# Performance work log

Measured on AMD Instinct MI355X. Metric: run time of the kernel, lower is better.

## Reference

```python
import jax, jax.numpy as jnp
import numpy as np

B, T, F, V, NTXT = 32, 1, 1, 729, 64
DIM, DIM_LLM = 1152, 4096
HEADS, DIM_HEAD, DEPTH, NUM_LATENTS, FF_MULT = 16, 96, 6, 64, 4
INNER = HEADS * DIM_HEAD
FF_INNER = DIM * FF_MULT
SCALE = DIM_HEAD ** -0.5


def _ln(x, w, b, eps=1e-5):
    mu = x.mean(-1, keepdims=True)
    var = ((x - mu) ** 2).mean(-1, keepdims=True)
    return (x - mu) * jax.lax.rsqrt(var + eps) * w + b


def setup_inputs() -> dict:
    key = jax.random.key(0)
    ks = jax.random.split(key, 12)
    w = lambda k, shape: jax.random.normal(k, shape, dtype=jnp.float32) * 0.02
    return {
        "x": jax.random.normal(ks[0], (B, T, F, V, DIM), dtype=jnp.float32),
        "text_embeds": jax.random.normal(ks[1], (B, NTXT, DIM_LLM), dtype=jnp.float32),
        "latents": jax.random.normal(ks[2], (NUM_LATENTS, DIM), dtype=jnp.float32),
        "txt_w1": w(ks[3], (DIM_LLM, DIM)),
        "txt_b1": jnp.zeros((DIM,), jnp.float32),
        "txt_w2": w(ks[4], (DIM, DIM)),
        "txt_b2": jnp.zeros((DIM,), jnp.float32),
        "nm_w": jnp.ones((DEPTH, DIM), jnp.float32),
        "nm_b": jnp.zeros((DEPTH, DIM), jnp.float32),
        "nl_w": jnp.ones((DEPTH, DIM), jnp.float32),
        "nl_b": jnp.zeros((DEPTH, DIM), jnp.float32),
        "Wq": w(ks[5], (DEPTH, DIM, INNER)),
        "Wkv": w(ks[6], (DEPTH, DIM, 2 * INNER)),
        "Wo": w(ks[7], (DEPTH, INNER, DIM)),
        "ffln_w": jnp.ones((DEPTH, DIM), jnp.float32),
        "ffln_b": jnp.zeros((DEPTH, DIM), jnp.float32),
        "ff_w1": w(ks[8], (DEPTH, DIM, FF_INNER)),
        "ff_w2": w(ks[9], (DEPTH, FF_INNER, DIM)),
        "out_ln_w": jnp.ones((DIM,), jnp.float32),
        "out_ln_b": jnp.zeros((DIM,), jnp.float32),
    }


def reference(x, text_embeds, latents, txt_w1, txt_b1, txt_w2, txt_b2,
              nm_w, nm_b, nl_w, nl_b, Wq, Wkv, Wo,
              ffln_w, ffln_b, ff_w1, ff_w2, out_ln_w, out_ln_b):
    b, t, f, v, d = x.shape
    xf = x.reshape(b, t, f * v, d)  # (b, T, F*v, D)
    # text_projection: Linear -> GELU -> Linear
    txt = jax.nn.gelu(text_embeds @ txt_w1 + txt_b1, approximate=False) @ txt_w2 + txt_b2
    lat = jnp.broadcast_to(latents, (b, t, NUM_LATENTS, d))
    lat = jnp.concatenate(
        [lat, jnp.broadcast_to(txt[:, None], (b, t, txt.shape[1], d))], axis=2)
    n2 = lat.shape[2]
    for i in range(DEPTH):
        # PerceiverAttention
        xm = _ln(xf, nm_w[i], nm_b[i])
        lm = _ln(lat, nl_w[i], nl_b[i])
        q = (lm @ Wq[i]).reshape(b, t, n2, HEADS, DIM_HEAD)
        kv = jnp.concatenate([xm, lm], axis=2) @ Wkv[i]
        k, v_ = jnp.split(kv, 2, axis=-1)
        nk = k.shape[2]
        k = k.reshape(b, t, nk, HEADS, DIM_HEAD)
        v_ = v_.reshape(b, t, nk, HEADS, DIM_HEAD)
        sim = jnp.einsum('btihd,btjhd->bthij', q * SCALE, k)
        attn = jax.nn.softmax(sim, axis=-1)  # stable softmax == amax subtract + softmax
        out = jnp.einsum('bthij,btjhd->btihd', attn, v_).reshape(b, t, n2, INNER) @ Wo[i]
        lat = out + lat
        # FeedForward: LN -> Linear -> GELU -> Linear, residual
        lat = jax.nn.gelu(_ln(lat, ffln_w[i], ffln_b[i]) @ ff_w1[i],
                          approximate=False) @ ff_w2[i] + lat
    lat = lat[:, :, :NUM_LATENTS, :]
    return _ln(lat, out_ln_w, out_ln_b)
```

## Files before the change

### kernel.cpp

```cpp
#include <hip/hip_runtime.h>
#include <hip/hip_bf16.h>
#include <math.h>


typedef __attribute__((ext_vector_type(4))) float f32x4;
typedef __attribute__((ext_vector_type(8))) short bf16x8;
typedef unsigned int u32;

#define DEV __device__ __forceinline__

DEV float bf2f(short s){ union{u32 u; float f;} v; v.u = ((u32)(unsigned short)s) << 16; return v.f; }
DEV short f2bf(float f){
  union{float f; u32 u;} v; v.f = f;
  u32 r = (v.u + 0x7FFFu + ((v.u >> 16) & 1u)) >> 16;
  return (short)r;
}

DEV u32 lds_off(const short* p){
  return (u32)(uintptr_t)(__attribute__((address_space(3))) const short*)p;
}
template<int OFF>
DEV bf16x8 dsro(u32 addr){
  bf16x8 r;
  asm volatile("ds_read_b128 %0, %1 offset:%2" : "=v"(r) : "v"(addr), "i"(OFF));
  return r;
}

template<int GELU, int BIAS, int OUTF32, int CMAP, int KSPLIT>
__global__ __launch_bounds__(512, 4)
void gemm_v2(const short* __restrict__ A, const short* __restrict__ Bm,
             void* __restrict__ Cv, short* __restrict__ C2,
             const float* __restrict__ bias,
             int K, int lda, int ldb, int ldc,
             int Mvalid, int NBmax, int Nwrite)
{
  __shared__ __align__(16) short LDS[36864];

  int Mb = gridDim.x;
  int nwg = gridDim.x * gridDim.y;
  int bid = blockIdx.y * gridDim.x + blockIdx.x;
  int m0, n0;
  if ((Mb & 7) == 0){
    int mslab = Mb >> 3;
    int c = bid & 7, s = bid >> 3;
    int ml = s % mslab, nl = s / mslab;
    m0 = (c*mslab + ml) * 128;
    n0 = nl * 256;
  } else if ((nwg & 7) == 0){
    int chunk = nwg >> 3;
    int b2 = (bid & 7)*chunk + (bid >> 3);
    int by = b2 / Mb;
    m0 = (b2 - by*Mb) * 128;
    n0 = by * 256;
  } else {
    m0 = blockIdx.x * 128;
    n0 = blockIdx.y * 256;
  }
  int kzoff = KSPLIT ? (int)blockIdx.z * K : 0;

  int tid = threadIdx.x, lane = tid & 63, w = tid >> 6;
  int wr = w >> 2, wc = w & 3;
  int rsel = lane & 15, g4 = lane >> 4;

  int sl = lane >> 3;
  int l  = (lane & 7) ^ sl;
  int lc = (l & 3) * 8;
  int lh = l >> 2;
  const short* gA;
  { int r = m0 + w*8 + sl + lh*64; if (r > Mvalid-1) r = Mvalid-1;
    gA = A + (long)r*lda + lc + kzoff; }
  const short* gB0;
  { int r = n0 + w*8 + sl + lh*128; if (r > NBmax-1) r = NBmax-1;
    gB0 = Bm + (long)r*ldb + lc + kzoff; }
  const short* gB1;
  { int r = n0 + 64 + w*8 + sl + lh*128; if (r > NBmax-1) r = NBmax-1;
    gB1 = Bm + (long)r*ldb + lc + kzoff; }
  char* dA  = (char*)LDS + w*1024;
  char* dB0 = (char*)LDS + 8192  + w*1024;
  char* dB1 = (char*)LDS + 16384 + w*1024;

#define GLDS(src, dst) __builtin_amdgcn_global_load_lds( \
      (const __attribute__((address_space(1))) u32*)(src), \
      (__attribute__((address_space(3))) u32*)(dst), 16, 0, 0)
#define STAGE(bo, tau) do { \
    int kb = (tau)*32; \
    GLDS(gA  + kb, dA  + (bo)); \
    GLDS(gB0 + kb, dB0 + (bo)); \
    GLDS(gB1 + kb, dB1 + (bo)); \
  } while(0)

  u32 base = lds_off(LDS);
  u32 aAddr = base + (u32)(rsel*128 + (((wr*4 + g4) ^ (rsel & 7))*16));
  u32 bAddr = base + 8192u
            + (u32)(((wc & 1)*64 + rsel)*128 + ((((wc >> 1)*4 + g4) ^ (rsel & 7))*16));

  int nt = K >> 5;

  f32x4 acc[4][4];
#pragma unroll
  for (int i=0;i<4;i++)
#pragma unroll
    for (int j=0;j<4;j++) acc[i][j] = (f32x4){0.f,0.f,0.f,0.f};

  STAGE(0u, 0);
  if (nt > 1) STAGE(24576u, 1);

  u32 boCur = 0;
#pragma unroll 1
  for (int t=0; t<nt; ++t){
    if (t == nt-1) { asm volatile("s_waitcnt vmcnt(0)" ::: "memory"); }
    else           { asm volatile("s_waitcnt vmcnt(3)" ::: "memory"); }
    asm volatile("s_barrier" ::: "memory");
    u32 aa = aAddr + boCur, bb = bAddr + boCur;
    bf16x8 af[4], bfr[4];
    af[0]  = dsro<0>(aa);    af[1]  = dsro<2048>(aa);
    af[2]  = dsro<4096>(aa); af[3]  = dsro<6144>(aa);
    bfr[0] = dsro<0>(bb);    bfr[1] = dsro<2048>(bb);
    bfr[2] = dsro<4096>(bb); bfr[3] = dsro<6144>(bb);
    if (t+2 < nt){
      u32 boN2 = boCur + 49152u; if (boN2 >= 73728u) boN2 -= 73728u;
      STAGE(boN2, t+2);
    }
    asm volatile("s_waitcnt lgkmcnt(0)" ::: "memory");
    __builtin_amdgcn_sched_barrier(0);
    __builtin_amdgcn_s_setprio(1);
#pragma unroll
    for (int mi=0; mi<4; mi++)
#pragma unroll
      for (int nn=0; nn<4; nn++)
        acc[mi][nn] = __builtin_amdgcn_mfma_f32_16x16x32_bf16(af[mi], bfr[nn], acc[mi][nn], 0, 0, 0);
    __builtin_amdgcn_s_setprio(0);
    boCur += 24576u; if (boCur == 73728u) boCur = 0;
  }
#undef STAGE
#undef GLDS

  int cq = g4 * 4;
  int csel = rsel;
#pragma unroll
  for (int mi=0; mi<4; mi++){
#pragma unroll
    for (int nn=0; nn<4; nn++){
#pragma unroll
      for (int j=0; j<4; j++){
        int gm = m0 + wr*64 + mi*16 + cq + j;
        int gn = n0 + wc*64 + nn*16 + csel;
        if (gm < Mvalid && gn < Nwrite){
          float v = acc[mi][nn][j];
          if (BIAS) v += bias[gn];
          if (GELU) v = 0.5f*v*(1.0f + erff(v*0.70710678118654752f));
          if (CMAP == 0){
            long off = (long)gm*ldc + gn;
            if (KSPLIT) off += (long)blockIdx.z * ((long)Mvalid * ldc);
            if (OUTF32) ((float*)Cv)[off] = v;
            else        ((short*)Cv)[off] = f2bf(v);
          } else if (CMAP == 1){
            int bb2 = gm / 729;
            int jj = gm - bb2*729;
            ((short*)Cv)[((long)bb2*857 + jj)*3072 + gn] = f2bf(v);
          } else {
            if (gn < 1536){
              ((short*)Cv)[(long)gm*1536 + gn] = f2bf(v * 0.1020620726159657f);
            } else {
              int bb2 = gm >> 7, jj = gm & 127;
              C2[((long)bb2*857 + 729 + jj)*3072 + (gn - 1536)] = f2bf(v);
            }
          }
        }
      }
    }
  }
}

__global__ __launch_bounds__(512, 4)
void gemm_qkvx(const short* __restrict__ lm, const short* __restrict__ xnorm,
               const short* __restrict__ wTq, const short* __restrict__ wTx,
               short* __restrict__ qb, short* __restrict__ kv,
               const float* __restrict__ biasL)
{
  __shared__ __align__(16) short LDS[36864];

  int bid = blockIdx.x;
  int which = (bid >= 576);
  const short* A; const short* Bm;
  int m0, n0, Mvalid, NBmax;
  if (!which){
    int mslab = 4;
    int c = bid & 7, s = bid >> 3;
    m0 = (c*mslab + s % mslab) * 128;
    n0 = (s / mslab) * 256;
    A = lm; Bm = wTq; Mvalid = 4096; NBmax = 4608;
  } else {
    int local = bid - 576;
    int mslab = 23;
    int c = local & 7, s = local >> 3;
    m0 = (c*mslab + s % mslab) * 128;
    n0 = (s / mslab) * 256;
    A = xnorm; Bm = wTx; Mvalid = 23328; NBmax = 3072;
  }

  int tid = threadIdx.x, lane = tid & 63, w = tid >> 6;
  int wr = w >> 2, wc = w & 3;
  int rsel = lane & 15, g4 = lane >> 4;

  int sl = lane >> 3;
  int l  = (lane & 7) ^ sl;
  int lc = (l & 3) * 8;
  int lh = l >> 2;
  const short* gA;
  { int r = m0 + w*8 + sl + lh*64; if (r > Mvalid-1) r = Mvalid-1;
    gA = A + (long)r*1152 + lc; }
  const short* gB0;
  { int r = n0 + w*8 + sl + lh*128; if (r > NBmax-1) r = NBmax-1;
    gB0 = Bm + (long)r*1152 + lc; }
  const short* gB1;
  { int r = n0 + 64 + w*8 + sl + lh*128; if (r > NBmax-1) r = NBmax-1;
    gB1 = Bm + (long)r*1152 + lc; }
  char* dA  = (char*)LDS + w*1024;
  char* dB0 = (char*)LDS + 8192  + w*1024;
  char* dB1 = (char*)LDS + 16384 + w*1024;

#define GLDS(src, dst) __builtin_amdgcn_global_load_lds( \
      (const __attribute__((address_space(1))) u32*)(src), \
      (__attribute__((address_space(3))) u32*)(dst), 16, 0, 0)
#define STAGE(bo, tau) do { \
    int kb = (tau)*32; \
    GLDS(gA  + kb, dA  + (bo)); \
    GLDS(gB0 + kb, dB0 + (bo)); \
    GLDS(gB1 + kb, dB1 + (bo)); \
  } while(0)

  u32 base = lds_off(LDS);
  u32 aAddr = base + (u32)(rsel*128 + (((wr*4 + g4) ^ (rsel & 7))*16));
  u32 bAddr = base + 8192u
            + (u32)(((wc & 1)*64 + rsel)*128 + ((((wc >> 1)*4 + g4) ^ (rsel & 7))*16));

  const int nt = 36;

  f32x4 acc[4][4];
#pragma unroll
  for (int i=0;i<4;i++)
#pragma unroll
    for (int j=0;j<4;j++) acc[i][j] = (f32x4){0.f,0.f,0.f,0.f};

  STAGE(0u, 0);
  STAGE(24576u, 1);

  u32 boCur = 0;
#pragma unroll 1
  for (int t=0; t<nt; ++t){
    if (t == nt-1) { asm volatile("s_waitcnt vmcnt(0)" ::: "memory"); }
    else           { asm volatile("s_waitcnt vmcnt(3)" ::: "memory"); }
    asm volatile("s_barrier" ::: "memory");
    u32 aa = aAddr + boCur, bb = bAddr + boCur;
    bf16x8 af[4], bfr[4];
    af[0]  = dsro<0>(aa);    af[1]  = dsro<2048>(aa);
    af[2]  = dsro<4096>(aa); af[3]  = dsro<6144>(aa);
    bfr[0] = dsro<0>(bb);    bfr[1] = dsro<2048>(bb);
    bfr[2] = dsro<4096>(bb); bfr[3] = dsro<6144>(bb);
    if (t+2 < nt){
      u32 boN2 = boCur + 49152u; if (boN2 >= 73728u) boN2 -= 73728u;
      STAGE(boN2, t+2);
    }
    asm volatile("s_waitcnt lgkmcnt(0)" ::: "memory");
    __builtin_amdgcn_sched_barrier(0);
    __builtin_amdgcn_s_setprio(1);
#pragma unroll
    for (int mi=0; mi<4; mi++)
#pragma unroll
      for (int nn=0; nn<4; nn++)
        acc[mi][nn] = __builtin_amdgcn_mfma_f32_16x16x32_bf16(af[mi], bfr[nn], acc[mi][nn], 0, 0, 0);
    __builtin_amdgcn_s_setprio(0);
    boCur += 24576u; if (boCur == 73728u) boCur = 0;
  }
#undef STAGE
#undef GLDS

  int cq = g4 * 4;
  int csel = rsel;
#pragma unroll
  for (int mi=0; mi<4; mi++){
#pragma unroll
    for (int nn=0; nn<4; nn++){
#pragma unroll
      for (int j=0; j<4; j++){
        int gm = m0 + wr*64 + mi*16 + cq + j;
        int gn = n0 + wc*64 + nn*16 + csel;
        if (!which){
          if (gm < 4096 && gn < 4608){
            float v = acc[mi][nn][j];
            if (gn < 1536){
              qb[(long)gm*1536 + gn] = f2bf(v * 0.1020620726159657f);
            } else {
              int bb2 = gm >> 7, jj = gm & 127;
              kv[((long)bb2*857 + 729 + jj)*3072 + (gn - 1536)] = f2bf(v);
            }
          }
        } else {
          if (gm < 23328 && gn < 3072){
            float v = acc[mi][nn][j] + biasL[gn];
            int bb2 = gm / 729;
            int jj = gm - bb2*729;
            kv[((long)bb2*857 + jj)*3072 + gn] = f2bf(v);
          }
        }
      }
    }
  }
}

__global__ __launch_bounds__(256)
void red2_ln(float* __restrict__ lat, const float* __restrict__ p, long n,
             short* __restrict__ lm, const float* __restrict__ w,
             const float* __restrict__ b)
{
  const int D = 1152;
  int r = blockIdx.x;
  long rb = (long)r*D;
  int tid = threadIdx.x;
  float s1=0.f, s2=0.f;
  float xv[5];
#pragma unroll
  for (int t=0;t<5;t++){
    int i = tid + t*256;
    float v = 0.f;
    if (i < D){
      v = lat[rb+i] + p[rb+i] + p[n+rb+i];
      lat[rb+i] = v;
    }
    xv[t] = v; s1 += v; s2 += v*v;
  }
  if (!w) return;
#pragma unroll
  for (int o=32;o;o>>=1){ s1 += __shfl_xor(s1,o); s2 += __shfl_xor(s2,o); }
  __shared__ float red[8];
  int wid = tid>>6, lane = tid&63;
  if (lane==0){ red[wid]=s1; red[4+wid]=s2; }
  __syncthreads();
  s1 = red[0]+red[1]+red[2]+red[3];
  s2 = red[4]+red[5]+red[6]+red[7];
  float mu = s1 / D;
  float var = s2 / D - mu*mu;
  float rs = rsqrtf(var + 1e-5f);
#pragma unroll
  for (int t=0;t<5;t++){
    int i = tid + t*256;
    if (i >= D) break;
    lm[rb+i] = f2bf((xv[t]-mu)*rs*w[i] + b[i]);
  }
}

__global__ __launch_bounds__(256)
void flash_attn(const short* __restrict__ qb, const short* __restrict__ kv,
                short* __restrict__ attn)
{
  __shared__ short Kt[96][104];
  __shared__ short Vs[96][104];
  __shared__ short Pb[4][32][104];
  __shared__ float FAC[128];

  int z = blockIdx.x;
  int b = z >> 4, h = z & 15;
  int tid = threadIdx.x;
  int lane = tid & 63;
  int w = tid >> 6;
  int l15 = lane & 15, g4 = lane >> 4;

  bf16x8 qf[2][3];
#pragma unroll
  for (int n=0;n<2;n++)
#pragma unroll
    for (int kf=0;kf<3;kf++)
      qf[n][kf] = *(const bf16x8*)&qb[((long)(b*128 + w*32 + n*16 + l15))*1536
                                     + h*96 + kf*32 + g4*8];

  f32x4 acc[2][6];
#pragma unroll
  for (int i=0;i<2;i++)
#pragma unroll
    for (int j=0;j<6;j++) acc[i][j] = (f32x4){0.f,0.f,0.f,0.f};
  float m_run[2] = {-1e30f, -1e30f};
  float l_run[2] = {0.f, 0.f};

  const short* kvb = kv + (long)b*857*3072 + h*96;
  const short* vvb = kvb + 1536;

  for (int t=0; t<9; ++t){
    int k0 = t*96;
    for (int c = tid; c < 1152; c += 256){
      int r = c / 12;
      int c12 = c - r*12;
      int key = k0 + r; if (key > 856) key = 856;
      *(bf16x8*)&Kt[r][c12*8] = *(const bf16x8*)&kvb[(long)key*3072 + c12*8];
      bf16x8 vv = *(const bf16x8*)&vvb[(long)key*3072 + c12*8];
#pragma unroll
      for (int j=0;j<8;j++) Vs[c12*8 + j][r] = ((short*)&vv)[j];
    }
    __syncthreads();

    f32x4 st[6][2];
#pragma unroll
    for (int m=0;m<6;m++){ st[m][0]=(f32x4){0,0,0,0}; st[m][1]=(f32x4){0,0,0,0}; }
#pragma unroll
    for (int kf=0;kf<3;kf++){
      bf16x8 af[6];
#pragma unroll
      for (int m=0;m<6;m++) af[m] = *(const bf16x8*)&Kt[m*16 + l15][kf*32 + g4*8];
#pragma unroll
      for (int m=0;m<6;m++){
        st[m][0] = __builtin_amdgcn_mfma_f32_16x16x32_bf16(af[m], qf[0][kf], st[m][0], 0,0,0);
        st[m][1] = __builtin_amdgcn_mfma_f32_16x16x32_bf16(af[m], qf[1][kf], st[m][1], 0,0,0);
      }
    }

    if (k0 + 96 > 857){
#pragma unroll
      for (int m=0;m<6;m++)
#pragma unroll
        for (int j=0;j<4;j++){
          if (k0 + m*16 + g4*4 + j > 856){ st[m][0][j] = -1e30f; st[m][1][j] = -1e30f; }
        }
    }

#pragma unroll
    for (int n=0;n<2;n++){
      float mx = -1e30f;
#pragma unroll
      for (int m=0;m<6;m++)
#pragma unroll
        for (int j=0;j<4;j++) mx = fmaxf(mx, st[m][n][j]);
      mx = fmaxf(mx, __shfl_xor(mx, 16));
      mx = fmaxf(mx, __shfl_xor(mx, 32));
      float mn = fmaxf(m_run[n], mx);
      float f  = __expf(m_run[n] - mn);
      m_run[n] = mn;
      float s = 0.f;
#pragma unroll
      for (int m=0;m<6;m++)
#pragma unroll
        for (int j=0;j<4;j++){
          float e = __expf(st[m][n][j] - mn);
          st[m][n][j] = e; s += e;
        }
      s += __shfl_xor(s, 16);
      s += __shfl_xor(s, 32);
      l_run[n] = l_run[n]*f + s;
      if (g4 == 0) FAC[w*32 + n*16 + l15] = f;
    }

#pragma unroll
    for (int m=0;m<6;m++)
#pragma unroll
      for (int n=0;n<2;n++){
        short4 pk;
        pk.x = f2bf(st[m][n][0]); pk.y = f2bf(st[m][n][1]);
        pk.z = f2bf(st[m][n][2]); pk.w = f2bf(st[m][n][3]);
        *(short4*)&Pb[w][n*16 + l15][m*16 + g4*4] = pk;
      }

    {
      float4 fj0 = *(const float4*)&FAC[w*32 +  0 + g4*4];
      float4 fj1 = *(const float4*)&FAC[w*32 + 16 + g4*4];
#pragma unroll
      for (int nn=0;nn<6;nn++){
        acc[0][nn][0] *= fj0.x; acc[0][nn][1] *= fj0.y;
        acc[0][nn][2] *= fj0.z; acc[0][nn][3] *= fj0.w;
        acc[1][nn][0] *= fj1.x; acc[1][nn][1] *= fj1.y;
        acc[1][nn][2] *= fj1.z; acc[1][nn][3] *= fj1.w;
      }
    }

#pragma unroll
    for (int kf=0;kf<3;kf++){
      bf16x8 pa0 = *(const bf16x8*)&Pb[w][ 0 + l15][kf*32 + g4*8];
      bf16x8 pa1 = *(const bf16x8*)&Pb[w][16 + l15][kf*32 + g4*8];
#pragma unroll
      for (int nn=0;nn<6;nn++){
        bf16x8 vb = *(const bf16x8*)&Vs[nn*16 + l15][kf*32 + g4*8];
        acc[0][nn] = __builtin_amdgcn_mfma_f32_16x16x32_bf16(pa0, vb, acc[0][nn], 0,0,0);
        acc[1][nn] = __builtin_amdgcn_mfma_f32_16x16x32_bf16(pa1, vb, acc[1][nn], 0,0,0);
      }
    }
    __syncthreads();
  }

  if (g4 == 0){
    FAC[w*32 +  0 + l15] = 1.0f / l_run[0];
    FAC[w*32 + 16 + l15] = 1.0f / l_run[1];
  }
  float4 li0 = *(const float4*)&FAC[w*32 +  0 + g4*4];
  float4 li1 = *(const float4*)&FAC[w*32 + 16 + g4*4];
  float li[2][4] = {{li0.x,li0.y,li0.z,li0.w},{li1.x,li1.y,li1.z,li1.w}};
#pragma unroll
  for (int mo=0;mo<2;mo++)
#pragma unroll
    for (int nn=0;nn<6;nn++)
#pragma unroll
      for (int j=0;j<4;j++){
        int q = w*32 + mo*16 + g4*4 + j;
        int d = nn*16 + l15;
        attn[((long)(b*128+q))*1536 + h*96 + d] = f2bf(acc[mo][nn][j]*li[mo][j]);
      }
}

template<int GELU, int BIAS, int RES, int OUTF32>
__global__ __launch_bounds__(256)
void gemm_t(const short* __restrict__ A, const short* __restrict__ B,
            void* __restrict__ C, const float* __restrict__ bias,
            const float* __restrict__ res,
            int K, int lda, int ldb, int ldc,
            int Mvalid, int NBmax, int Nwrite,
            int zdiv, long sA1, long sA2, long sB1, long sB2, long sC1, long sC2,
            float scale)
{
  __shared__ __align__(16) short As[2][128*32];
  __shared__ __align__(16) short Bs[2][128*32];

  int z = blockIdx.z;
  int zq = z / zdiv, zr = z - zq*zdiv;
  const short* Ab = A + zq*sA1 + zr*sA2;
  const short* Bb = B + zq*sB1 + zr*sB2;
  long cOff = zq*sC1 + zr*sC2;
  int m0 = blockIdx.y * 128;
  int n0 = blockIdx.x * 128;
  int tid = threadIdx.x;
  int lane = tid & 63;
  int w = tid >> 6;
  int wm = (w >> 1) * 64, wn = (w & 1) * 64;

  int sr = lane >> 2;
  int sc = (lane & 3) * 8;
  int ar0 = m0 + w*32 + sr;
  int br0 = n0 + w*32 + sr;

  int raA0 = ar0;      if (raA0 > Mvalid-1) raA0 = Mvalid-1;
  int raA1 = ar0 + 16; if (raA1 > Mvalid-1) raA1 = Mvalid-1;
  int rbB0 = br0;      if (rbB0 > NBmax-1) rbB0 = NBmax-1;
  int rbB1 = br0 + 16; if (rbB1 > NBmax-1) rbB1 = NBmax-1;
  const short* gA0 = Ab + (long)raA0*lda + sc;
  const short* gA1 = Ab + (long)raA1*lda + sc;
  const short* gB0 = Bb + (long)rbB0*ldb + sc;
  const short* gB1 = Bb + (long)rbB1*ldb + sc;
  int ldsRow0 = (w*32)*32;
  int ldsRow1 = (w*32 + 16)*32;

  f32x4 acc[4][4];
#pragma unroll
  for (int i=0;i<4;i++)
#pragma unroll
    for (int j=0;j<4;j++) acc[i][j] = (f32x4){0.f,0.f,0.f,0.f};

  auto stage = [&](int buf, int kb){
    __builtin_amdgcn_global_load_lds(
        (const __attribute__((address_space(1))) u32*)(gA0 + kb),
        (__attribute__((address_space(3))) u32*)(&As[buf][ldsRow0]), 16, 0, 0);
    __builtin_amdgcn_global_load_lds(
        (const __attribute__((address_space(1))) u32*)(gA1 + kb),
        (__attribute__((address_space(3))) u32*)(&As[buf][ldsRow1]), 16, 0, 0);
    __builtin_amdgcn_global_load_lds(
        (const __attribute__((address_space(1))) u32*)(gB0 + kb),
        (__attribute__((address_space(3))) u32*)(&Bs[buf][ldsRow0]), 16, 0, 0);
    __builtin_amdgcn_global_load_lds(
        (const __attribute__((address_space(1))) u32*)(gB1 + kb),
        (__attribute__((address_space(3))) u32*)(&Bs[buf][ldsRow1]), 16, 0, 0);
  };

  int nt = K >> 5;
  stage(0, 0);
  __syncthreads();

  int kq = (lane >> 4) * 8;
  int rsel = lane & 15;
  int cur = 0;
  for (int t = 0; t < nt; ++t){
    if (t + 1 < nt) stage(cur ^ 1, (t+1)*32);

    bf16x8 af[4], bfr[4];
#pragma unroll
    for (int m=0;m<4;m++) af[m]  = *(const bf16x8*)&As[cur][(wm + m*16 + rsel)*32 + kq];
#pragma unroll
    for (int n=0;n<4;n++) bfr[n] = *(const bf16x8*)&Bs[cur][(wn + n*16 + rsel)*32 + kq];
#pragma unroll
    for (int m=0;m<4;m++)
#pragma unroll
      for (int n=0;n<4;n++)
        acc[m][n] = __builtin_amdgcn_mfma_f32_16x16x32_bf16(af[m], bfr[n], acc[m][n], 0, 0, 0);

    __syncthreads();
    cur ^= 1;
  }

  int cq = (lane >> 4) * 4;
  int csel = lane & 15;
#pragma unroll
  for (int m=0;m<4;m++){
#pragma unroll
    for (int n=0;n<4;n++){
#pragma unroll
      for (int j=0;j<4;j++){
        int gm = m0 + wm + m*16 + cq + j;
        int gn = n0 + wn + n*16 + csel;
        if (gm < Mvalid && gn < Nwrite){
          float v = acc[m][n][j] * scale;
          if (BIAS) v += bias[gn];
          if (GELU) v = 0.5f*v*(1.0f + erff(v*0.70710678118654752f));
          long off = cOff + (long)gm*ldc + gn;
          if (OUTF32){
            float rv = RES ? res[off] : 0.0f;
            ((float*)C)[off] = v + rv;
          } else {
            ((short*)C)[off] = f2bf(v);
          }
        }
      }
    }
  }
}

__global__ __launch_bounds__(256)
void convT(const float* __restrict__ in, short* __restrict__ out,
           int K, int N, const float* __restrict__ s)
{
  __shared__ float tile[32][33];
  int kb = blockIdx.y*32, nb = blockIdx.x*32;
  int tx = threadIdx.x & 31, ty = threadIdx.x >> 5;
  for (int i = ty; i < 32; i += 8){
    int k = kb + i, n = nb + tx;
    float v = 0.f;
    if (k < K && n < N){ v = in[(long)k*N + n]; if (s) v *= s[k]; }
    tile[i][tx] = v;
  }
  __syncthreads();
  for (int i = ty; i < 32; i += 8){
    int n = nb + i, k = kb + tx;
    if (n < N && k < K) out[(long)n*K + k] = f2bf(tile[tx][i]);
  }
}

__global__ __launch_bounds__(256)
void convT_qkv(const float* __restrict__ Wq, const float* __restrict__ Wkv,
               const float* __restrict__ s,
               short* __restrict__ outQ, short* __restrict__ outKx,
               short* __restrict__ outK)
{
  __shared__ float tile[32][33];
  __shared__ float sv[32];
  int b = blockIdx.x;
  int tx = threadIdx.x & 31, ty = threadIdx.x >> 5;
  if (b < 1728){
    int bx = b % 48, byy = b / 48;
    int kb = byy*32, nb = bx*32;
    for (int i = ty; i < 32; i += 8)
      tile[i][tx] = Wq[(long)(kb + i)*1536 + nb + tx];
    __syncthreads();
    for (int i = ty; i < 32; i += 8)
      outQ[(long)(nb + i)*1152 + kb + tx] = f2bf(tile[tx][i]);
  } else {
    int b2 = b - 1728;
    int bx = b2 % 96, byy = b2 / 96;
    int kb = byy*32, nb = bx*32;
    if (threadIdx.x < 32) sv[threadIdx.x] = s[kb + threadIdx.x];
    for (int i = ty; i < 32; i += 8)
      tile[i][tx] = Wkv[(long)(kb + i)*3072 + nb + tx];
    __syncthreads();
    for (int i = ty; i < 32; i += 8){
      float v = tile[tx][i];
      long o = (long)(nb + i)*1152 + kb + tx;
      outK[o]  = f2bf(v);
      outKx[o] = f2bf(v * sv[tx]);
    }
  }
}

__global__ __launch_bounds__(256)
void convT_ffo(const float* __restrict__ Wo, const float* __restrict__ fw1,
               const float* __restrict__ fw2,
               short* __restrict__ outWo, short* __restrict__ outF1,
               short* __restrict__ outF2)
{
  __shared__ float tile[32][33];
  int b = blockIdx.x;
  int tx = threadIdx.x & 31, ty = threadIdx.x >> 5;
  const float* in; short* out; int K, N, kb, nb;
  if (b < 1728){
    in = Wo; out = outWo; K = 1536; N = 1152;
    nb = (b % 36)*32; kb = (b / 36)*32;
  } else if (b < 6912){
    int b2 = b - 1728;
    in = fw1; out = outF1; K = 1152; N = 4608;
    nb = (b2 % 144)*32; kb = (b2 / 144)*32;
  } else {
    int b3 = b - 6912;
    in = fw2; out = outF2; K = 4608; N = 1152;
    nb = (b3 % 36)*32; kb = (b3 / 36)*32;
  }
  for (int i = ty; i < 32; i += 8)
    tile[i][tx] = in[(long)(kb + i)*N + nb + tx];
  __syncthreads();
  for (int i = ty; i < 32; i += 8)
    out[(long)(nb + i)*K + kb + tx] = f2bf(tile[tx][i]);
}

__global__ __launch_bounds__(256)
void biasfold6(const float* __restrict__ Wkv, const float* __restrict__ nm_b,
               float* __restrict__ outb)
{
  int L = blockIdx.y;
  int n = blockIdx.x*256 + threadIdx.x;
  const float* W = Wkv + (size_t)L*1152*3072;
  const float* bvec = nm_b + L*1152;
  float s = 0.f;
  for (int k=0;k<1152;k++) s += bvec[k]*W[(long)k*3072 + n];
  outb[L*3072 + n] = s;
}

__global__ __launch_bounds__(256)
void cvt_bf16x4(const float* __restrict__ in, short* __restrict__ o, long n)
{
  long i = ((long)blockIdx.x*256 + threadIdx.x)*4;
  if (i >= n) return;
  float4 v = *(const float4*)(in + i);
  short4 s4;
  s4.x = f2bf(v.x); s4.y = f2bf(v.y); s4.z = f2bf(v.z); s4.w = f2bf(v.w);
  *(short4*)&o[i] = s4;
}

__global__ __launch_bounds__(256)
void latcopy(const float* __restrict__ latents, float* __restrict__ lat)
{
  int idx = blockIdx.x*256 + threadIdx.x;
  int d = idx % 1152; int j = (idx / 1152) % 64; int b = idx / (1152*64);
  lat[((long)b*128 + j)*1152 + d] = latents[j*1152 + d];
}

template<int OUTF32>
__global__ __launch_bounds__(256)
void ln_k(const float* __restrict__ in, void* __restrict__ outp,
          const float* __restrict__ w, const float* __restrict__ b,
          int grpSel, int grpStride)
{
  const int D = 1152;
  int r = blockIdx.x;
  long ir = (long)(r / grpSel)*grpStride + (r % grpSel);
  const float* x = in + ir*D;
  int tid = threadIdx.x;
  float s1=0.f, s2=0.f;
  float xv[5];
#pragma unroll
  for (int t=0;t<5;t++){
    int i = tid + t*256;
    xv[t] = (i < D) ? x[i] : 0.f;
    s1 += xv[t]; s2 += xv[t]*xv[t];
  }
#pragma unroll
  for (int o=32;o;o>>=1){ s1 += __shfl_xor(s1,o); s2 += __shfl_xor(s2,o); }
  __shared__ float red[8];
  int wid = tid>>6, lane = tid&63;
  if (lane==0){ red[wid]=s1; red[4+wid]=s2; }
  __syncthreads();
  s1 = red[0]+red[1]+red[2]+red[3];
  s2 = red[4]+red[5]+red[6]+red[7];
  float mu = s1 / D;
  float var = s2 / D - mu*mu;
  float rs = rsqrtf(var + 1e-5f);
#pragma unroll
  for (int t=0;t<5;t++){
    int i = tid + t*256;
    if (i >= D) break;
    float v = (xv[t]-mu)*rs;
    if (w) v = v*w[i] + b[i];
    if (OUTF32) ((float*)outp)[(long)r*D + i] = v;
    else        ((short*)outp)[(long)r*D + i] = f2bf(v);
  }
}


extern "C" void kernel_launch(void* const* d_in, const int* in_sizes, int n_in,
                              void* d_out, int out_size, void* d_ws, size_t ws_size,
                              hipStream_t stream)
{
  const float* x      = (const float*)d_in[0];
  const float* tein   = (const float*)d_in[1];
  const float* lat0   = (const float*)d_in[2];
  const float* txt_w1 = (const float*)d_in[3];
  const float* txt_b1 = (const float*)d_in[4];
  const float* txt_w2 = (const float*)d_in[5];
  const float* txt_b2 = (const float*)d_in[6];
  const float* nm_w   = (const float*)d_in[7];
  const float* nm_b   = (const float*)d_in[8];
  const float* nl_w   = (const float*)d_in[9];
  const float* nl_b   = (const float*)d_in[10];
  const float* Wq     = (const float*)d_in[11];
  const float* Wkv    = (const float*)d_in[12];
  const float* Wo     = (const float*)d_in[13];
  const float* ffln_w = (const float*)d_in[14];
  const float* ffln_b = (const float*)d_in[15];
  const float* ff_w1  = (const float*)d_in[16];
  const float* ff_w2  = (const float*)d_in[17];
  const float* oln_w  = (const float*)d_in[18];
  const float* oln_b  = (const float*)d_in[19];
  float* out = (float*)d_out;
  (void)in_sizes; (void)n_in; (void)out_size; (void)ws_size;

  char* base = (char*)d_ws;
  size_t off = 0;
  auto alloc = [&](size_t bytes)->char*{
    char* r = base + off;
    off += (bytes + 255) & ~(size_t)255;
    return r;
  };
  short* wT    = (short*)alloc(4608ULL*1152*2);
  short* wTx   = (short*)alloc(3072ULL*1152*2);
  short* wTo   = (short*)alloc(1152ULL*1536*2);
  short* wTf1  = (short*)alloc(4608ULL*1152*2);
  short* wTf2  = (short*)alloc(1152ULL*4608*2);
  float* biasf = (float*)alloc(6*3072*4);
  float* ppart = (float*)alloc(2ULL*4096*1152*4);
  short* xnorm = (short*)alloc(23328ULL*1152*2);
  float* lat   = (float*)alloc(4096ULL*1152*4);
  short* lm    = (short*)alloc(4096ULL*1152*2);
  short* qb    = (short*)alloc(4096ULL*1536*2);
  short* kv    = (short*)alloc(27424ULL*3072*2);
  short* SP    = (short*)alloc(2048ULL*4096*2 + 2048ULL*1152*2);
  short* attn  = (short*)alloc(4096ULL*1536*2);
  short* ffh   = (short*)alloc(4096ULL*4608*2);
  short* txtin = SP;
  short* txth  = SP + 2048ULL*4096;

  cvt_bf16x4<<<8192,256,0,stream>>>(tein, txtin, 2048LL*4096);
  convT<<<dim3(36,128),256,0,stream>>>(txt_w1, wT, 4096, 1152, nullptr);
  gemm_t<1,1,0,0><<<dim3(9,16,1),256,0,stream>>>(txtin, wT, txth, txt_b1, nullptr,
      4096,4096,4096,1152, 2048,1152,1152, 1, 0,0,0,0,0,0, 1.f);
  convT<<<dim3(36,36),256,0,stream>>>(txt_w2, wT, 1152, 1152, nullptr);
  gemm_t<0,1,0,1><<<dim3(9,1,32),256,0,stream>>>(txth, wT, lat + 64*1152, txt_b2, nullptr,
      1152,1152,1152,1152, 64,1152,1152, 1, 64L*1152,0, 0,0, 128L*1152,0, 1.f);
  latcopy<<<9216,256,0,stream>>>(lat0, lat);

  ln_k<0><<<23328,256,0,stream>>>(x, xnorm, nullptr, nullptr, 1<<28, 0);
  ln_k<0><<<4096,256,0,stream>>>(lat, lm, nl_w, nl_b, 1<<28, 0);
  biasfold6<<<dim3(12,6),256,0,stream>>>(Wkv, nm_b, biasf);

  for (int L=0; L<6; L++){
    const float* WqL  = Wq    + (size_t)L*1152*1536;
    const float* WkvL = Wkv   + (size_t)L*1152*3072;
    const float* WoL  = Wo    + (size_t)L*1536*1152;
    const float* fw1  = ff_w1 + (size_t)L*1152*4608;
    const float* fw2  = ff_w2 + (size_t)L*4608*1152;
    int Ln = (L+1 < 6) ? (L+1) : 5;

    convT_qkv<<<5184,256,0,stream>>>(WqL, WkvL, nm_w + L*1152,
        wT, wTx, wT + 1536*1152);

    gemm_qkvx<<<2784,512,0,stream>>>(lm, xnorm, wT, wTx, qb, kv, biasf + L*3072);

    flash_attn<<<512,256,0,stream>>>(qb, kv, attn);

    convT_ffo<<<12096,256,0,stream>>>(WoL, fw1, fw2, wTo, wTf1, wTf2);

    gemm_v2<0,0,1,0,1><<<dim3(32,5,2),512,0,stream>>>(attn, wTo, ppart, nullptr, nullptr,
        768,1536,1536,1152, 4096, 1152, 1152);
    red2_ln<<<4096,256,0,stream>>>(lat, ppart, 4096L*1152, lm,
        ffln_w + L*1152, ffln_b + L*1152);

    gemm_v2<1,0,0,0,0><<<dim3(32,18),512,0,stream>>>(lm, wTf1, ffh, nullptr, nullptr,
        1152,1152,1152,4608, 4096, 4608, 4608);
    gemm_v2<0,0,1,0,1><<<dim3(32,5,2),512,0,stream>>>(ffh, wTf2, ppart, nullptr, nullptr,
        2304,4608,4608,1152, 4096, 1152, 1152);
    red2_ln<<<4096,256,0,stream>>>(lat, ppart, 4096L*1152, lm,
        (L+1 < 6) ? (nl_w + Ln*1152) : nullptr, nl_b + Ln*1152);
  }

  ln_k<1><<<2048,256,0,stream>>>(lat, out, oln_w, oln_b, 64, 128);
}
```

Measured before the change: 3.631 ms.

## Fuse next-layer QKV weight transpose into FF2 split-K GEMM launch

Adds a combined kernel that runs the FF2 split-K GEMM (320 blocks) and, in extra blocks of the same grid, transposes and converts the next layer's Wq/Wkv weights to bf16, including the norm-scaled copy. The standalone per-layer convT_qkv launch is removed and layer 0's transpose moves before the loop. This hides the transpose work in the GEMM's tail and cuts launch overhead. The risk is that the transpose blocks compete with GEMM blocks for CUs and LDS, because each block reserves the GEMM's large shared allocation. On the last layer the kernel redundantly re-transposes layer 5's weights.

```diff
diff --git a/kernel.cpp b/kernel.cpp
--- a/kernel.cpp
+++ b/kernel.cpp
@@ -309,6 +309,151 @@
   }
 }
 
+__global__ __launch_bounds__(512, 4)
+void gemm_f2t(const short* __restrict__ ffh, const short* __restrict__ wTf2,
+              float* __restrict__ ppart,
+              const float* __restrict__ WqN, const float* __restrict__ WkvN,
+              const float* __restrict__ sN,
+              short* __restrict__ outQ, short* __restrict__ outKx,
+              short* __restrict__ outK)
+{
+  __shared__ __align__(16) short LDS[36864];
+  __shared__ float tile[32][33];
+  __shared__ float sv[32];
+
+  int bid = blockIdx.x;
+  if (bid >= 320){
+    int b = bid - 320;
+    int tx = threadIdx.x & 31, ty = threadIdx.x >> 5;
+    if (b < 1728){
+      int bx = b % 48, byy = b / 48;
+      int kb = byy*32, nb = bx*32;
+      for (int i = ty; i < 32; i += 16)
+        tile[i][tx] = WqN[(long)(kb + i)*1536 + nb + tx];
+      __syncthreads();
+      for (int i = ty; i < 32; i += 16)
+        outQ[(long)(nb + i)*1152 + kb + tx] = f2bf(tile[tx][i]);
+    } else {
+      int b2 = b - 1728;
+      int bx = b2 % 96, byy = b2 / 96;
+      int kb = byy*32, nb = bx*32;
+      if (threadIdx.x < 32) sv[threadIdx.x] = sN[kb + threadIdx.x];
+      for (int i = ty; i < 32; i += 16)
+        tile[i][tx] = WkvN[(long)(kb + i)*3072 + nb + tx];
+      __syncthreads();
+      for (int i = ty; i < 32; i += 16){
+        float v = tile[tx][i];
+        long o = (long)(nb + i)*1152 + kb + tx;
+        outK[o]  = f2bf(v);
+        outKx[o] = f2bf(v * sv[tx]);
+      }
+    }
+    return;
+  }
+
+  int bz  = bid / 160;
+  int lin = bid - bz*160;
+  int c = lin & 7, s = lin >> 3;
+  int m0 = (c*4 + (s & 3)) * 128;
+  int n0 = (s >> 2) * 256;
+  int kzoff = bz * 2304;
+
+  int tid = threadIdx.x, lane = tid & 63, w = tid >> 6;
+  int wr = w >> 2, wc = w & 3;
+  int rsel = lane & 15, g4 = lane >> 4;
+
+  int sl = lane >> 3;
+  int l  = (lane & 7) ^ sl;
+  int lc = (l & 3) * 8;
+  int lh = l >> 2;
+  const short* gA;
+  { int r = m0 + w*8 + sl + lh*64; if (r > 4095) r = 4095;
+    gA = ffh + (long)r*4608 + lc + kzoff; }
+  const short* gB0;
+  { int r = n0 + w*8 + sl + lh*128; if (r > 1151) r = 1151;
+    gB0 = wTf2 + (long)r*4608 + lc + kzoff; }
+  const short* gB1;
+  { int r = n0 + 64 + w*8 + sl + lh*128; if (r > 1151) r = 1151;
+    gB1 = wTf2 + (long)r*4608 + lc + kzoff; }
+  char* dA  = (char*)LDS + w*1024;
+  char* dB0 = (char*)LDS + 8192  + w*1024;
+  char* dB1 = (char*)LDS + 16384 + w*1024;
+
+#define GLDS(src, dst) __builtin_amdgcn_global_load_lds( \
+      (const __attribute__((address_space(1))) u32*)(src), \
+      (__attribute__((address_space(3))) u32*)(dst), 16, 0, 0)
+#define STAGE(bo, tau) do { \
+    int kb = (tau)*32; \
+    GLDS(gA  + kb, dA  + (bo)); \
+    GLDS(gB0 + kb, dB0 + (bo)); \
+    GLDS(gB1 + kb, dB1 + (bo)); \
+  } while(0)
+
+  u32 base = lds_off(LDS);
+  u32 aAddr = base + (u32)(rsel*128 + (((wr*4 + g4) ^ (rsel & 7))*16));
+  u32 bAddr = base + 8192u
+            + (u32)(((wc & 1)*64 + rsel)*128 + ((((wc >> 1)*4 + g4) ^ (rsel & 7))*16));
+
+  const int nt = 72;
+
+  f32x4 acc[4][4];
+#pragma unroll
+  for (int i=0;i<4;i++)
+#pragma unroll
+    for (int j=0;j<4;j++) acc[i][j] = (f32x4){0.f,0.f,0.f,0.f};
+
+  STAGE(0u, 0);
+  STAGE(24576u, 1);
+
+  u32 boCur = 0;
+#pragma unroll 1
+  for (int t=0; t<nt; ++t){
+    if (t == nt-1) { asm volatile("s_waitcnt vmcnt(0)" ::: "memory"); }
+    else           { asm volatile("s_waitcnt vmcnt(3)" ::: "memory"); }
+    asm volatile("s_barrier" ::: "memory");
+    u32 aa = aAddr + boCur, bb = bAddr + boCur;
+    bf16x8 af[4], bfr[4];
+    af[0]  = dsro<0>(aa);    af[1]  = dsro<2048>(aa);
+    af[2]  = dsro<4096>(aa); af[3]  = dsro<6144>(aa);
+    bfr[0] = dsro<0>(bb);    bfr[1] = dsro<2048>(bb);
+    bfr[2] = dsro<4096>(bb); bfr[3] = dsro<6144>(bb);
+    if (t+2 < nt){
+      u32 boN2 = boCur + 49152u; if (boN2 >= 73728u) boN2 -= 73728u;
+      STAGE(boN2, t+2);
+    }
+    asm volatile("s_waitcnt lgkmcnt(0)" ::: "memory");
+    __builtin_amdgcn_sched_barrier(0);
+    __builtin_amdgcn_s_setprio(1);
+#pragma unroll
+    for (int mi=0; mi<4; mi++)
+#pragma unroll
+      for (int nn=0; nn<4; nn++)
+        acc[mi][nn] = __builtin_amdgcn_mfma_f32_16x16x32_bf16(af[mi], bfr[nn], acc[mi][nn], 0, 0, 0);
+    __builtin_amdgcn_s_setprio(0);
+    boCur += 24576u; if (boCur == 73728u) boCur = 0;
+  }
+#undef STAGE
+#undef GLDS
+
+  int cq = g4 * 4;
+  int csel = rsel;
+  long zoff = (long)bz * (4096L*1152);
+#pragma unroll
+  for (int mi=0; mi<4; mi++){
+#pragma unroll
+    for (int nn=0; nn<4; nn++){
+#pragma unroll
+      for (int j=0; j<4; j++){
+        int gm = m0 + wr*64 + mi*16 + cq + j;
+        int gn = n0 + wc*64 + nn*16 + csel;
+        if (gm < 4096 && gn < 1152){
+          ppart[zoff + (long)gm*1152 + gn] = acc[mi][nn][j];
+        }
+      }
+    }
+  }
+}
+
 __global__ __launch_bounds__(256)
 void red2_ln(float* __restrict__ lat, const float* __restrict__ p, long n,
              short* __restrict__ lm, const float* __restrict__ w,
@@ -839,18 +984,14 @@
   ln_k<0><<<23328,256,0,stream>>>(x, xnorm, nullptr, nullptr, 1<<28, 0);
   ln_k<0><<<4096,256,0,stream>>>(lat, lm, nl_w, nl_b, 1<<28, 0);
   biasfold6<<<dim3(12,6),256,0,stream>>>(Wkv, nm_b, biasf);
+  convT_qkv<<<5184,256,0,stream>>>(Wq, Wkv, nm_w, wT, wTx, wT + 1536*1152);
 
   for (int L=0; L<6; L++){
-    const float* WqL  = Wq    + (size_t)L*1152*1536;
-    const float* WkvL = Wkv   + (size_t)L*1152*3072;
     const float* WoL  = Wo    + (size_t)L*1536*1152;
     const float* fw1  = ff_w1 + (size_t)L*1152*4608;
     const float* fw2  = ff_w2 + (size_t)L*4608*1152;
     int Ln = (L+1 < 6) ? (L+1) : 5;
 
-    convT_qkv<<<5184,256,0,stream>>>(WqL, WkvL, nm_w + L*1152,
-        wT, wTx, wT + 1536*1152);
-
     gemm_qkvx<<<2784,512,0,stream>>>(lm, xnorm, wT, wTx, qb, kv, biasf + L*3072);
 
     flash_attn<<<512,256,0,stream>>>(qb, kv, attn);
@@ -864,8 +1005,11 @@
 
     gemm_v2<1,0,0,0,0><<<dim3(32,18),512,0,stream>>>(lm, wTf1, ffh, nullptr, nullptr,
         1152,1152,1152,4608, 4096, 4608, 4608);
-    gemm_v2<0,0,1,0,1><<<dim3(32,5,2),512,0,stream>>>(ffh, wTf2, ppart, nullptr, nullptr,
-        2304,4608,4608,1152, 4096, 1152, 1152);
+
+    gemm_f2t<<<5504,512,0,stream>>>(ffh, wTf2, ppart,
+        Wq + (size_t)Ln*1152*1536, Wkv + (size_t)Ln*1152*3072, nm_w + Ln*1152,
+        wT, wTx, wT + 1536*1152);
+
     red2_ln<<<4096,256,0,stream>>>(lat, ppart, 4096L*1152, lm,
         (L+1 < 6) ? (nl_w + Ln*1152) : nullptr, nl_b + Ln*1152);
   }
```

New measurement: 3.590 ms. No clear change (-1.1%).
